# Optimization experiments

Measured on AMD Instinct MI355X. Metric: run time of the kernel, lower is better.

## Reference

```python
import jax, jax.numpy as jnp
import numpy as np

GAMMA = 1.0   # focal exponent
THETA = 1.0   # boundary weight scale
SIGMA = 1.0   # distance decay
EPS = 1e-8
BIG = 1e10    # 'no boundary point in this column' sentinel


def _boundary(mask):
    # mask: [H,W] bool. Boundary = foreground pixel with a 4-neighbor background
    # (image border counts as background via zero padding).
    p = jnp.pad(mask, 1)
    inner = (p[1:-1, 1:-1] & p[:-2, 1:-1] & p[2:, 1:-1]
             & p[1:-1, :-2] & p[1:-1, 2:])
    return mask & ~inner


def _sqdist(mask):
    # Exact squared Euclidean distance transform to the True pixels of mask,
    # via separable two-pass min:  d2(x,y) = min_{y'} [ (y-y')^2 + min_{x':mask[x',y']} (x-x')^2 ]
    H, W = mask.shape
    xs = jnp.arange(H, dtype=jnp.float32)
    dx2 = (xs[:, None] - xs[None, :]) ** 2                      # [H,H]
    col = jnp.where(mask, 0.0, BIG)                             # [H,W]
    g = jnp.min(dx2[:, :, None] + col[None, :, :], axis=1)      # [H,W] min over x'
    ys = jnp.arange(W, dtype=jnp.float32)
    dy2 = (ys[:, None] - ys[None, :]) ** 2                      # [W,W] (y,y')
    return jnp.min(g[:, None, :] + dy2[None, :, :], axis=2)     # [H,W] min over y'


def _weight_map(prob, label):
    # prob, label: [H,W] float
    ib = _boundary(prob > 0.5)    # predicted-image boundary pixels
    lb = _boundary(label > 0.5)   # label boundary pixels
    d_to_ib = jnp.sqrt(_sqdist(ib))   # distance of every pixel to nearest image boundary
    d_to_lb = jnp.sqrt(_sqdist(lb))   # distance of every pixel to nearest label boundary
    w = (1.0
         + THETA * jnp.where(lb, jnp.exp(-d_to_ib / SIGMA), 0.0)
         + THETA * jnp.where(ib, jnp.exp(-d_to_lb / SIGMA), 0.0))
    return w


def setup_inputs() -> dict:
    key = jax.random.key(0)
    k1, k2 = jax.random.split(key)
    B, H, W = 8, 256, 256
    inp = jax.random.normal(k1, (B, H, W), dtype=jnp.float32)
    target = (jax.random.uniform(k2, (B, H, W)) < 0.5).astype(jnp.float32)
    return {"input": inp, "target": target}


def reference(input, target):
    probs = jax.nn.sigmoid(input)
    # weight maps are built from detached CPU copies in the original -> stop_gradient
    w = jax.lax.stop_gradient(jax.vmap(_weight_map)(probs, target))
    loss = w * (-(1.0 - probs) ** GAMMA * target * jnp.log(probs + EPS)
                - probs ** GAMMA * (1.0 - target) * jnp.log(1.0 - probs + EPS))
    return jnp.mean(loss)
```

## Files before the change

kernel.cpp:

```cpp
#include <hip/hip_runtime.h>

#define HW_BIG   1e10f
#define LOSS_EPS 1e-8f

typedef unsigned long long u64;

__device__ __forceinline__ int row_nearest(const u64* rm, int y) {
    const int yw = y >> 6, yb = y & 63;
    int dd = 32768;
    u64 w = rm[yw] & (~0ULL >> (63 - yb));
    int j = yw;
    while (w == 0 && j > 0) w = rm[--j];
    if (w) dd = y - (j * 64 + 63 - __builtin_clzll(w));
    u64 w2 = rm[yw] & (~0ULL << yb);
    int j2 = yw;
    while (w2 == 0 && j2 < 3) w2 = rm[++j2];
    if (w2) { int du = (j2 * 64 + __builtin_ctzll(w2)) - y; dd = min(dd, du); }
    return dd;
}

__global__ void k_masks(const float* __restrict__ inp,
                        const float* __restrict__ tgt,
                        u64* __restrict__ rows_bib,
                        u64* __restrict__ rows_blb,
                        u64* __restrict__ rows_ml) {
    __shared__ u64 V[6][4];
    __shared__ u64 T[6][4];
    const int tid = threadIdx.x;
    const int img = blockIdx.x >> 6;
    const int r0  = (blockIdx.x & 63) * 4;
    const int r   = tid >> 8;
    const int y   = tid & 255;
    const int w   = y >> 6;
    const float* ip = inp + (size_t)img * 65536;
    const float* tp = tgt + (size_t)img * 65536;

    const int x = r0 + r;
    bool vb = ip[x * 256 + y] > 0.0f;
    bool tb = tp[x * 256 + y] > 0.5f;
    u64 bv = __ballot(vb);
    u64 bt = __ballot(tb);
    if ((y & 63) == 0) { V[r][w] = bv; T[r][w] = bt; }

    if (tid < 256) {
        const int xh = r0 - 1;
        bool hv = (xh >= 0) && (ip[xh * 256 + y] > 0.0f);
        bool ht = (xh >= 0) && (tp[xh * 256 + y] > 0.5f);
        u64 a = __ballot(hv), b = __ballot(ht);
        if ((y & 63) == 0) { V[4][w] = a; T[4][w] = b; }
    } else if (tid < 512) {
        const int xh = r0 + 4;
        bool hv = (xh < 256) && (ip[xh * 256 + y] > 0.0f);
        bool ht = (xh < 256) && (tp[xh * 256 + y] > 0.5f);
        u64 a = __ballot(hv), b = __ballot(ht);
        if ((y & 63) == 0) { V[5][w] = a; T[5][w] = b; }
    }
    __syncthreads();

    if (tid < 32) {
        const int rr = (tid >> 2) & 3;
        const int j  = tid & 3;
        const bool isT = tid >= 16;
        const u64 (*M)[4] = isT ? T : V;
        u64 own = M[rr][j];
        u64 up  = (rr == 0) ? M[4][j] : M[rr - 1][j];
        u64 dn  = (rr == 3) ? M[5][j] : M[rr + 1][j];
        u64 lf  = (own << 1) | ((j > 0) ? (M[rr][j - 1] >> 63) : 0ULL);
        u64 rt  = (own >> 1) | ((j < 3) ? (M[rr][j + 1] << 63) : 0ULL);
        u64 bnd = own & ~(up & dn & lf & rt);
        const size_t o = ((size_t)img * 256 + (r0 + rr)) * 4 + j;
        if (!isT) rows_bib[o] = bnd;
        else      { rows_blb[o] = bnd; rows_ml[o] = own; }
    }
}

__global__ void k_dt_loss(const float* __restrict__ inp,
                          const u64* __restrict__ rows_bib,
                          const u64* __restrict__ rows_blb,
                          const u64* __restrict__ rows_ml,
                          float* __restrict__ partials) {
    __shared__ u64 Mib[1024];
    __shared__ u64 Mlb[1024];
    __shared__ u64 Mml[1024];
    __shared__ float G1[256][8];
    __shared__ float G2[256][8];
    __shared__ float wsum[16];
    const int tid = threadIdx.x;
    const int img = blockIdx.x >> 5;
    const int y0  = (blockIdx.x & 31) * 8;
    const int x   = tid >> 2;
    const int yq  = tid & 3;
    const int ya  = y0 + yq;
    const int yb  = ya + 4;

    const size_t mbase = (size_t)img * 1024;
    Mib[tid] = rows_bib[mbase + tid];
    Mlb[tid] = rows_blb[mbase + tid];
    Mml[tid] = rows_ml[mbase + tid];
    const float va = inp[((size_t)img * 256 + x) * 256 + ya];
    const float vb = inp[((size_t)img * 256 + x) * 256 + yb];
    __syncthreads();

    const int ywa = ya >> 6, yba = ya & 63;
    const int ywb = yb >> 6, ybb = yb & 63;
    const bool fibA = (Mib[x * 4 + ywa] >> yba) & 1;
    const bool flbA = (Mlb[x * 4 + ywa] >> yba) & 1;
    const float tA  = ((Mml[x * 4 + ywa] >> yba) & 1) ? 1.0f : 0.0f;
    const bool fibB = (Mib[x * 4 + ywb] >> ybb) & 1;
    const bool flbB = (Mlb[x * 4 + ywb] >> ybb) & 1;
    const float tB  = ((Mml[x * 4 + ywb] >> ybb) & 1) ? 1.0f : 0.0f;

    {
        const int d1a = row_nearest(&Mib[x * 4], ya);
        const int d2a = row_nearest(&Mlb[x * 4], ya);
        const int d1b = row_nearest(&Mib[x * 4], yb);
        const int d2b = row_nearest(&Mlb[x * 4], yb);
        G1[x][yq]     = (d1a > 255) ? HW_BIG : (float)(d1a * d1a);
        G2[x][yq]     = (d2a > 255) ? HW_BIG : (float)(d2a * d2a);
        G1[x][yq + 4] = (d1b > 255) ? HW_BIG : (float)(d1b * d1b);
        G2[x][yq + 4] = (d2b > 255) ? HW_BIG : (float)(d2b * d2b);
    }
    __syncthreads();

    float m1a = flbA ? G1[x][yq] : 0.0f;
    float m2a = fibA ? G2[x][yq] : 0.0f;
    for (int d = 1; d < 256; ++d) {
        const float fd2 = (float)(d * d);
        if (fd2 >= m1a && fd2 >= m2a) break;
        const int xl = x - d;
        if (xl >= 0)  { m1a = fminf(m1a, G1[xl][yq] + fd2); m2a = fminf(m2a, G2[xl][yq] + fd2); }
        const int xr = x + d;
        if (xr < 256) { m1a = fminf(m1a, G1[xr][yq] + fd2); m2a = fminf(m2a, G2[xr][yq] + fd2); }
    }
    float m1b = flbB ? G1[x][yq + 4] : 0.0f;
    float m2b = fibB ? G2[x][yq + 4] : 0.0f;
    for (int d = 1; d < 256; ++d) {
        const float fd2 = (float)(d * d);
        if (fd2 >= m1b && fd2 >= m2b) break;
        const int xl = x - d;
        if (xl >= 0)  { m1b = fminf(m1b, G1[xl][yq + 4] + fd2); m2b = fminf(m2b, G2[xl][yq + 4] + fd2); }
        const int xr = x + d;
        if (xr < 256) { m1b = fminf(m1b, G1[xr][yq + 4] + fd2); m2b = fminf(m2b, G2[xr][yq + 4] + fd2); }
    }

    const float pa = 1.0f / (1.0f + __expf(-va));
    float wA = 1.0f;
    if (flbA) wA += __expf(-sqrtf(m1a));
    if (fibA) wA += __expf(-sqrtf(m2a));
    float lossA = wA * (-(1.0f - pa) * tA * __logf(pa + LOSS_EPS)
                        - pa * (1.0f - tA) * __logf(1.0f - pa + LOSS_EPS));

    const float pb = 1.0f / (1.0f + __expf(-vb));
    float wB = 1.0f;
    if (flbB) wB += __expf(-sqrtf(m1b));
    if (fibB) wB += __expf(-sqrtf(m2b));
    float lossB = wB * (-(1.0f - pb) * tB * __logf(pb + LOSS_EPS)
                        - pb * (1.0f - tB) * __logf(1.0f - pb + LOSS_EPS));

    float s = lossA + lossB;
#pragma unroll
    for (int off = 32; off > 0; off >>= 1) s += __shfl_down(s, off, 64);
    if ((tid & 63) == 0) wsum[tid >> 6] = s;
    __syncthreads();
    if (tid == 0) {
        float bs = 0.0f;
#pragma unroll
        for (int i = 0; i < 16; ++i) bs += wsum[i];
        partials[blockIdx.x] = bs;
    }
}

__global__ void k_reduce(const float* __restrict__ partials, int n,
                         float* __restrict__ out, double inv_count) {
    __shared__ double sw[4];
    const int tid = threadIdx.x;
    double s = 0.0;
    for (int i = tid; i < n; i += 256) s += (double)partials[i];
#pragma unroll
    for (int off = 32; off > 0; off >>= 1) s += __shfl_down(s, off, 64);
    const int lane = tid & 63, wv = tid >> 6;
    if (lane == 0) sw[wv] = s;
    __syncthreads();
    if (tid == 0) out[0] = (float)(((sw[0] + sw[1]) + (sw[2] + sw[3])) * inv_count);
}

extern "C" void kernel_launch(void* const* d_in, const int* in_sizes, int n_in,
                              void* d_out, int out_size, void* d_ws, size_t ws_size,
                              hipStream_t stream) {
    const float* inp = (const float*)d_in[0];
    const float* tgt = (const float*)d_in[1];
    float* out = (float*)d_out;

    const int total = in_sizes[0];
    const int nimg  = total / 65536;
    const int nblk1 = nimg * 64;
    const int nblk2 = nimg * 32;

    char* ws = (char*)d_ws;
    u64*   rows_bib = (u64*)ws;
    u64*   rows_blb = rows_bib + (size_t)nimg * 1024;
    u64*   rows_ml  = rows_blb + (size_t)nimg * 1024;
    float* parts    = (float*)(rows_ml + (size_t)nimg * 1024);

    k_masks  <<<nblk1, 1024, 0, stream>>>(inp, tgt, rows_bib, rows_blb, rows_ml);
    k_dt_loss<<<nblk2, 1024, 0, stream>>>(inp, rows_bib, rows_blb, rows_ml, parts);
    k_reduce <<<1,     256,  0, stream>>>(parts, nblk2, out, 1.0 / (double)total);
}
```

Baseline: 17.23 us.

## Move boundary extraction into distance-transform kernel; simplify mask kernel to ballots

The mask kernel now only ballots the thresholded input and target into bit rows, using small 256-thread blocks with no shared memory or halo loads. Boundary extraction (4-neighbour erosion) is moved into the distance/loss kernel, where each block rebuilds both boundary masks from the full image bitmaps in shared memory. This removes the halo reloads, the extra sync and one bitmap write/read from the first kernel. In exchange, every one of the 32 blocks per image repeats the boundary computation and adds another barrier.

```diff
diff --git a/kernel.cpp b/kernel.cpp
--- a/kernel.cpp
+++ b/kernel.cpp
@@ -21,67 +21,27 @@
 
 __global__ void k_masks(const float* __restrict__ inp,
                         const float* __restrict__ tgt,
-                        u64* __restrict__ rows_bib,
-                        u64* __restrict__ rows_blb,
-                        u64* __restrict__ rows_ml) {
-    __shared__ u64 V[6][4];
-    __shared__ u64 T[6][4];
-    const int tid = threadIdx.x;
-    const int img = blockIdx.x >> 6;
-    const int r0  = (blockIdx.x & 63) * 4;
-    const int r   = tid >> 8;
-    const int y   = tid & 255;
-    const int w   = y >> 6;
-    const float* ip = inp + (size_t)img * 65536;
-    const float* tp = tgt + (size_t)img * 65536;
-
-    const int x = r0 + r;
-    bool vb = ip[x * 256 + y] > 0.0f;
-    bool tb = tp[x * 256 + y] > 0.5f;
-    u64 bv = __ballot(vb);
-    u64 bt = __ballot(tb);
-    if ((y & 63) == 0) { V[r][w] = bv; T[r][w] = bt; }
-
-    if (tid < 256) {
-        const int xh = r0 - 1;
-        bool hv = (xh >= 0) && (ip[xh * 256 + y] > 0.0f);
-        bool ht = (xh >= 0) && (tp[xh * 256 + y] > 0.5f);
-        u64 a = __ballot(hv), b = __ballot(ht);
-        if ((y & 63) == 0) { V[4][w] = a; T[4][w] = b; }
-    } else if (tid < 512) {
-        const int xh = r0 + 4;
-        bool hv = (xh < 256) && (ip[xh * 256 + y] > 0.0f);
-        bool ht = (xh < 256) && (tp[xh * 256 + y] > 0.5f);
-        u64 a = __ballot(hv), b = __ballot(ht);
-        if ((y & 63) == 0) { V[5][w] = a; T[5][w] = b; }
-    }
-    __syncthreads();
-
-    if (tid < 32) {
-        const int rr = (tid >> 2) & 3;
-        const int j  = tid & 3;
-        const bool isT = tid >= 16;
-        const u64 (*M)[4] = isT ? T : V;
-        u64 own = M[rr][j];
-        u64 up  = (rr == 0) ? M[4][j] : M[rr - 1][j];
-        u64 dn  = (rr == 3) ? M[5][j] : M[rr + 1][j];
-        u64 lf  = (own << 1) | ((j > 0) ? (M[rr][j - 1] >> 63) : 0ULL);
-        u64 rt  = (own >> 1) | ((j < 3) ? (M[rr][j + 1] << 63) : 0ULL);
-        u64 bnd = own & ~(up & dn & lf & rt);
-        const size_t o = ((size_t)img * 256 + (r0 + rr)) * 4 + j;
-        if (!isT) rows_bib[o] = bnd;
-        else      { rows_blb[o] = bnd; rows_ml[o] = own; }
+                        u64* __restrict__ mv,
+                        u64* __restrict__ ml) {
+    const size_t gid = (size_t)blockIdx.x * 256 + threadIdx.x;
+    const bool vb = inp[gid] > 0.0f;
+    const bool tb = tgt[gid] > 0.5f;
+    const u64 bv = __ballot(vb);
+    const u64 bt = __ballot(tb);
+    if ((threadIdx.x & 63) == 0) {
+        mv[gid >> 6] = bv;
+        ml[gid >> 6] = bt;
     }
 }
 
 __global__ void k_dt_loss(const float* __restrict__ inp,
-                          const u64* __restrict__ rows_bib,
-                          const u64* __restrict__ rows_blb,
-                          const u64* __restrict__ rows_ml,
+                          const u64* __restrict__ mv,
+                          const u64* __restrict__ ml,
                           float* __restrict__ partials) {
-    __shared__ u64 Mib[1024];
-    __shared__ u64 Mlb[1024];
-    __shared__ u64 Mml[1024];
+    __shared__ u64 Mv[1024];
+    __shared__ u64 Ml[1024];
+    __shared__ u64 Bib[1024];
+    __shared__ u64 Blb[1024];
     __shared__ float G1[256][8];
     __shared__ float G2[256][8];
     __shared__ float wsum[16];
@@ -94,27 +54,43 @@
     const int yb  = ya + 4;
 
     const size_t mbase = (size_t)img * 1024;
-    Mib[tid] = rows_bib[mbase + tid];
-    Mlb[tid] = rows_blb[mbase + tid];
-    Mml[tid] = rows_ml[mbase + tid];
+    Mv[tid] = mv[mbase + tid];
+    Ml[tid] = ml[mbase + tid];
     const float va = inp[((size_t)img * 256 + x) * 256 + ya];
     const float vb = inp[((size_t)img * 256 + x) * 256 + yb];
     __syncthreads();
 
+    {
+        const int xr_ = tid >> 2, j = tid & 3;
+        u64 own = Mv[tid];
+        u64 up  = (xr_ > 0)   ? Mv[tid - 4] : 0ULL;
+        u64 dn  = (xr_ < 255) ? Mv[tid + 4] : 0ULL;
+        u64 lf  = (own << 1) | ((j > 0) ? (Mv[tid - 1] >> 63) : 0ULL);
+        u64 rt  = (own >> 1) | ((j < 3) ? (Mv[tid + 1] << 63) : 0ULL);
+        Bib[tid] = own & ~(up & dn & lf & rt);
+        own = Ml[tid];
+        up  = (xr_ > 0)   ? Ml[tid - 4] : 0ULL;
+        dn  = (xr_ < 255) ? Ml[tid + 4] : 0ULL;
+        lf  = (own << 1) | ((j > 0) ? (Ml[tid - 1] >> 63) : 0ULL);
+        rt  = (own >> 1) | ((j < 3) ? (Ml[tid + 1] << 63) : 0ULL);
+        Blb[tid] = own & ~(up & dn & lf & rt);
+    }
+    __syncthreads();
+
     const int ywa = ya >> 6, yba = ya & 63;
     const int ywb = yb >> 6, ybb = yb & 63;
-    const bool fibA = (Mib[x * 4 + ywa] >> yba) & 1;
-    const bool flbA = (Mlb[x * 4 + ywa] >> yba) & 1;
-    const float tA  = ((Mml[x * 4 + ywa] >> yba) & 1) ? 1.0f : 0.0f;
-    const bool fibB = (Mib[x * 4 + ywb] >> ybb) & 1;
-    const bool flbB = (Mlb[x * 4 + ywb] >> ybb) & 1;
-    const float tB  = ((Mml[x * 4 + ywb] >> ybb) & 1) ? 1.0f : 0.0f;
+    const bool fibA = (Bib[x * 4 + ywa] >> yba) & 1;
+    const bool flbA = (Blb[x * 4 + ywa] >> yba) & 1;
+    const float tA  = ((Ml[x * 4 + ywa] >> yba) & 1) ? 1.0f : 0.0f;
+    const bool fibB = (Bib[x * 4 + ywb] >> ybb) & 1;
+    const bool flbB = (Blb[x * 4 + ywb] >> ybb) & 1;
+    const float tB  = ((Ml[x * 4 + ywb] >> ybb) & 1) ? 1.0f : 0.0f;
 
     {
-        const int d1a = row_nearest(&Mib[x * 4], ya);
-        const int d2a = row_nearest(&Mlb[x * 4], ya);
-        const int d1b = row_nearest(&Mib[x * 4], yb);
-        const int d2b = row_nearest(&Mlb[x * 4], yb);
+        const int d1a = row_nearest(&Bib[x * 4], ya);
+        const int d2a = row_nearest(&Blb[x * 4], ya);
+        const int d1b = row_nearest(&Bib[x * 4], yb);
+        const int d2b = row_nearest(&Blb[x * 4], yb);
         G1[x][yq]     = (d1a > 255) ? HW_BIG : (float)(d1a * d1a);
         G2[x][yq]     = (d2a > 255) ? HW_BIG : (float)(d2a * d2a);
         G1[x][yq + 4] = (d1b > 255) ? HW_BIG : (float)(d1b * d1b);
@@ -193,16 +169,15 @@
 
     const int total = in_sizes[0];
     const int nimg  = total / 65536;
-    const int nblk1 = nimg * 64;
+    const int nblk1 = total / 256;
     const int nblk2 = nimg * 32;
 
     char* ws = (char*)d_ws;
-    u64*   rows_bib = (u64*)ws;
-    u64*   rows_blb = rows_bib + (size_t)nimg * 1024;
-    u64*   rows_ml  = rows_blb + (size_t)nimg * 1024;
-    float* parts    = (float*)(rows_ml + (size_t)nimg * 1024);
+    u64*   mv    = (u64*)ws;
+    u64*   ml    = mv + (size_t)nimg * 1024;
+    float* parts = (float*)(ml + (size_t)nimg * 1024);
 
-    k_masks  <<<nblk1, 1024, 0, stream>>>(inp, tgt, rows_bib, rows_blb, rows_ml);
-    k_dt_loss<<<nblk2, 1024, 0, stream>>>(inp, rows_bib, rows_blb, rows_ml, parts);
+    k_masks  <<<nblk1, 256,  0, stream>>>(inp, tgt, mv, ml);
+    k_dt_loss<<<nblk2, 1024, 0, stream>>>(inp, mv, ml, parts);
     k_reduce <<<1,     256,  0, stream>>>(parts, nblk2, out, 1.0 / (double)total);
 }
```

Result: no change. 17.35 us (+0.7%).
